# Kernel tuning notes

Hardware: AMD Instinct MI355X
Metric: run time of the kernel (lower is better)

## Reference

```python
import jax, jax.numpy as jnp
from jax import lax
import numpy as np

N, V, P, WE, PE, H, M = 512, 50000, 50, 100, 25, 256, 100
D = WE + PE  # 125, LSTM layer-0 input


def setup_inputs() -> dict:
    key = jax.random.key(0)
    ks = jax.random.split(key, 16)
    s = 0.05  # keep tanh/sigmoid in linear-ish range
    rn = lambda k, shape: jax.random.normal(k, shape, jnp.float32) * s
    return {
        "word_idx": jax.random.randint(ks[0], (N,), 0, V),
        "pos_idx": jax.random.randint(ks[1], (N,), 0, P),
        "word_emb": rn(ks[2], (V, WE)),
        "pos_emb": rn(ks[3], (P, PE)),
        "Wih0": rn(ks[4], (2, 4 * H, D)),
        "Whh0": rn(ks[5], (2, 4 * H, H)),
        "bih0": rn(ks[6], (2, 4 * H)),
        "bhh0": rn(ks[7], (2, 4 * H)),
        "Wih1": rn(ks[8], (2, 4 * H, 2 * H)),
        "Whh1": rn(ks[9], (2, 4 * H, H)),
        "bih1": rn(ks[10], (2, 4 * H)),
        "bhh1": rn(ks[11], (2, 4 * H)),
        "W1": rn(ks[12], (M, 4 * H)),
        "b1": rn(ks[13], (M,)),
        "W2": rn(ks[14], (1, M)),
        "b2": rn(ks[15], (1,)),
    }


def _lstm_dir(x, Wih, Whh, bih, bhh, reverse):
    # x: [n, d_in]; PyTorch gate order i, f, g, o
    Hh = Whh.shape[1]
    xp = jnp.flip(x, 0) if reverse else x
    pre = xp @ Wih.T + (bih + bhh)  # [n, 4H], input contribution precomputed

    def step(carry, p):
        h, c = carry
        g = p + h @ Whh.T
        i, f, gg, o = jnp.split(g, 4)
        c = jax.nn.sigmoid(f) * c + jax.nn.sigmoid(i) * jnp.tanh(gg)
        h = jax.nn.sigmoid(o) * jnp.tanh(c)
        return (h, c), h

    init = (jnp.zeros((Hh,), x.dtype), jnp.zeros((Hh,), x.dtype))
    _, hs = lax.scan(step, init, pre)
    return jnp.flip(hs, 0) if reverse else hs


def _bilstm_layer(x, Wih, Whh, bih, bhh):
    fwd = _lstm_dir(x, Wih[0], Whh[0], bih[0], bhh[0], False)
    bwd = _lstm_dir(x, Wih[1], Whh[1], bih[1], bhh[1], True)
    return jnp.concatenate([fwd, bwd], axis=-1)  # [n, 2H]


def reference(word_idx, pos_idx, word_emb, pos_emb,
              Wih0, Whh0, bih0, bhh0, Wih1, Whh1, bih1, bhh1,
              W1, b1, W2, b2):
    # embedding lookup + concat -> [n, D]
    embeds = jnp.concatenate([word_emb[word_idx], pos_emb[pos_idx]], axis=-1)
    h = _bilstm_layer(embeds, Wih0, Whh0, bih0, bhh0)   # [n, 2H]
    h = _bilstm_layer(h, Wih1, Whh1, bih1, bhh1)        # [n, 2H]
    # Pairwise MLP scorer: score[i, j] = W2 @ tanh(W1 @ cat(h_i, h_j) + b1) + b2
    # Split W1 so we never materialize the [n, n, 4H] concat tensor.
    Hd = h.shape[-1]
    a = h @ W1[:, :Hd].T   # [n, M] head part
    b = h @ W1[:, Hd:].T   # [n, M] dep part
    hid = jnp.tanh(a[:, None, :] + b[None, :, :] + b1)  # [n, n, M]
    scores = jnp.einsum('ijm,m->ij', hid, W2[0]) + b2[0]
    return scores
```

## Files before the change

### kernel.cpp

```cpp
#include <hip/hip_runtime.h>
#include <hip/hip_bf16.h>
#include <stdint.h>


typedef _Float16 f16x2 __attribute__((ext_vector_type(2)));

#define SCOPE_AGENT __HIP_MEMORY_SCOPE_AGENT
constexpr uint32_t SENT = 0x7FFF7FFFu;

__device__ __forceinline__ float fdot2f(uint32_t w, uint32_t h, float acc) {
#if __has_builtin(__builtin_amdgcn_fdot2)
  return __builtin_amdgcn_fdot2(__builtin_bit_cast(f16x2, w),
                                __builtin_bit_cast(f16x2, h), acc, false);
#else
  f16x2 a = __builtin_bit_cast(f16x2, w);
  f16x2 b = __builtin_bit_cast(f16x2, h);
  return acc + (float)a.x * (float)b.x + (float)a.y * (float)b.y;
#endif
}

__device__ __forceinline__ float fsigm(float x) { return 1.f / (1.f + __expf(-x)); }
__device__ __forceinline__ float ftanh(float x) {
  float e = __expf(2.f * x);
  return 1.f - 2.f / (e + 1.f);
}

constexpr size_t ALN(size_t x) { return (x + 1023) & ~(size_t)1023; }
constexpr size_t O_EX    = 0;
constexpr size_t SZ_EX   = 4ull * 512 * 128 * 4;
constexpr size_t O_WPK   = ALN(O_EX + SZ_EX);
constexpr size_t SZ_WPK  = 4ull * 128 * 1024 * 4;
constexpr size_t O_X0    = ALN(O_WPK + SZ_WPK);
constexpr size_t SZ_X0   = 512ull * 125 * 4;
constexpr size_t O_WTIH0 = ALN(O_X0 + SZ_X0);
constexpr size_t SZ_WTIH0 = 2ull * 128 * 1024 * 4;
constexpr size_t O_WTIH1 = ALN(O_WTIH0 + SZ_WTIH0);
constexpr size_t SZ_WTIH1 = 2ull * 512 * 1024 * 4;
constexpr size_t O_WTA   = ALN(O_WTIH1 + SZ_WTIH1);
constexpr size_t SZ_WTAB = 512ull * 100 * 4;
constexpr size_t O_WTB   = ALN(O_WTA + SZ_WTAB);
constexpr size_t O_PRE0  = ALN(O_WTB + SZ_WTAB);
constexpr size_t SZ_PRE  = 2ull * 512 * 1024 * 4;
constexpr size_t O_PRE1  = ALN(O_PRE0 + SZ_PRE);
constexpr size_t O_H0    = ALN(O_PRE1 + SZ_PRE);
constexpr size_t SZ_H    = 512ull * 512 * 4;
constexpr size_t O_H1    = ALN(O_H0 + SZ_H);
constexpr size_t O_AM    = ALN(O_H1 + SZ_H);
constexpr size_t O_BT    = ALN(O_AM + SZ_WTAB);


__global__ void k_init_ex(uint32_t* __restrict__ ex) {
  ex[(size_t)blockIdx.x * 256 + threadIdx.x] = SENT;
}

__global__ void k_embed(const int* __restrict__ wi, const int* __restrict__ pi,
                        const float* __restrict__ we, const float* __restrict__ pe,
                        float* __restrict__ x0) {
  int i = blockIdx.x, k = threadIdx.x;
  if (k < 100)      x0[i * 125 + k] = we[(size_t)wi[i] * 100 + k];
  else if (k < 125) x0[i * 125 + k] = pe[(size_t)pi[i] * 25 + (k - 100)];
}

__global__ void k_transpose(const float* __restrict__ src, int srcRows, int srcCols,
                            int colOff, int colCnt, int dstRows, float* __restrict__ dst) {
  __shared__ float tile[32][33];
  int k0 = blockIdx.x * 32, m0 = blockIdx.y * 32;
  int tx = threadIdx.x, ty = threadIdx.y;
#pragma unroll
  for (int i = 0; i < 4; i++) {
    int m = m0 + ty + i * 8, k = k0 + tx;
    float v = 0.f;
    if (m < srcRows && k < colCnt) v = src[(size_t)m * srcCols + colOff + k];
    tile[ty + i * 8][tx] = v;
  }
  __syncthreads();
#pragma unroll
  for (int i = 0; i < 4; i++) {
    int k = k0 + ty + i * 8, m = m0 + tx;
    if (k < dstRows && m < srcRows) dst[(size_t)k * srcRows + m] = tile[tx][ty + i * 8];
  }
}

__global__ void k_packwhh(const float* __restrict__ whh0, const float* __restrict__ whh1,
                          uint32_t* __restrict__ wpk) {
  int ld = blockIdx.x;
  int kp = blockIdx.y;
  int o  = threadIdx.x;
  const float* W = (ld < 2) ? (whh0 + (size_t)ld * 1024 * 256)
                            : (whh1 + (size_t)(ld - 2) * 1024 * 256);
  int b = o >> 9, t = o & 511;
  int gate = t >> 7, u = t & 127;
  int R = gate * 256 + b * 128 + u;
  f16x2 p;
  p.x = (_Float16)W[(size_t)R * 256 + 2 * kp];
  p.y = (_Float16)W[(size_t)R * 256 + 2 * kp + 1];
  wpk[(size_t)ld * 131072 + (size_t)kp * 1024 + o] = __builtin_bit_cast(uint32_t, p);
}

__global__ __launch_bounds__(256) void k_gemm(
    const float* __restrict__ X, const float* __restrict__ WT,
    const float* __restrict__ bias1, const float* __restrict__ bias2,
    float* __restrict__ out, int Mm, int Nn, int Kpad, int Kreal, int ldx,
    int flipX, int outT) {
  __shared__ float XS[32][64];
  int tid = threadIdx.x;
  int cl = tid & 63, rg = tid >> 6;
  int col = blockIdx.y * 64 + cl;
  int colr = (col < Nn) ? col : (Nn - 1);
  int row0 = blockIdx.x * 32;
  float acc[8];
#pragma unroll
  for (int r = 0; r < 8; r++) acc[r] = 0.f;
  for (int k0 = 0; k0 < Kpad; k0 += 64) {
#pragma unroll
    for (int ii = 0; ii < 8; ii++) {
      int idx = ii * 256 + tid;
      int r = idx >> 6, kk = idx & 63;
      int gr = row0 + r;
      int xr = flipX ? (Mm - 1 - gr) : gr;
      int k = k0 + kk;
      XS[r][kk] = (k < Kreal) ? X[(size_t)xr * ldx + k] : 0.f;
    }
    __syncthreads();
#pragma unroll 4
    for (int kk = 0; kk < 64; kk++) {
      float w = WT[(size_t)(k0 + kk) * Nn + colr];
#pragma unroll
      for (int r = 0; r < 8; r++) acc[r] += XS[rg * 8 + r][kk] * w;
    }
    __syncthreads();
  }
  if (col < Nn) {
    float bb = (bias1 ? bias1[col] : 0.f) + (bias2 ? bias2[col] : 0.f);
#pragma unroll
    for (int r = 0; r < 8; r++) {
      int gr = row0 + rg * 8 + r;
      float v = acc[r] + bb;
      if (outT) out[(size_t)col * Mm + gr] = v;
      else      out[(size_t)gr * Nn + col] = v;
    }
  }
}

__global__ __launch_bounds__(512, 2) void k_lstm(
    const float* __restrict__ preBase, const uint32_t* __restrict__ wpkL,
    float* __restrict__ hout, uint32_t* __restrict__ exL) {
  int d = blockIdx.x >> 1, b = blockIdx.x & 1;
  int t = threadIdx.x;
  int gate = t >> 7, u = t & 127;
  const float* pre = preBase + (size_t)d * 512 * 1024;
  const uint32_t* wsrc = wpkL + (size_t)d * 131072;
  uint32_t* ex = exL + (size_t)d * 512 * 128;

  __shared__ __align__(16) uint32_t h2[128];
  __shared__ float gl[512];
  __shared__ float hh[128];

  uint32_t w[128];
#pragma unroll
  for (int kp = 0; kp < 128; kp++) w[kp] = wsrc[(size_t)kp * 1024 + b * 512 + t];
  if (t < 128) h2[t] = 0u;
  float c = 0.f;
  const int RR = gate * 256 + b * 128 + u;
  __syncthreads();

  float pcur = pre[RR];
  for (int s = 0; s < 512; s++) {
    float pnext = (s < 511) ? pre[(size_t)(s + 1) * 1024 + RR] : 0.f;
    float a0 = pcur, a1 = 0.f, a2 = 0.f, a3 = 0.f;
    const uint4* h4 = (const uint4*)h2;
#pragma unroll
    for (int cc = 0; cc < 32; cc++) {
      uint4 hv = h4[cc];
      a0 = fdot2f(w[4 * cc + 0], hv.x, a0);
      a1 = fdot2f(w[4 * cc + 1], hv.y, a1);
      a2 = fdot2f(w[4 * cc + 2], hv.z, a2);
      a3 = fdot2f(w[4 * cc + 3], hv.w, a3);
    }
    gl[t] = (a0 + a1) + (a2 + a3);
    __syncthreads();
    if (t < 128) {
      float gi = gl[u], gf = gl[128 + u], gg = gl[256 + u], go = gl[384 + u];
      c = fsigm(gf) * c + fsigm(gi) * ftanh(gg);
      float h = fsigm(go) * ftanh(c);
      hh[u] = h;
      int pos = (d == 0) ? s : (511 - s);
      hout[(size_t)pos * 512 + d * 256 + b * 128 + u] = h;
    }
    __syncthreads();
    if (t < 64) {
      f16x2 p;
      p.x = (_Float16)hh[2 * t];
      p.y = (_Float16)hh[2 * t + 1];
      uint32_t pk = __builtin_bit_cast(uint32_t, p);
      h2[b * 64 + t] = pk;
      __hip_atomic_store(&ex[(size_t)s * 128 + b * 64 + t], pk,
                         __ATOMIC_RELAXED, SCOPE_AGENT);
      uint32_t q;
      do {
        q = __hip_atomic_load(&ex[(size_t)s * 128 + (b ^ 1) * 64 + t],
                              __ATOMIC_RELAXED, SCOPE_AGENT);
      } while (__any(q == SENT));
      h2[(b ^ 1) * 64 + t] = q;
    }
    pcur = pnext;
    __syncthreads();
  }
}

__global__ __launch_bounds__(512) void k_score(
    const float* __restrict__ am, const float* __restrict__ bT,
    const float* __restrict__ W2, const float* __restrict__ b2,
    float* __restrict__ out) {
  int i = blockIdx.x;
  int j = threadIdx.x;
  __shared__ float aL[100], w2L[100];
  if (j < 100) { aL[j] = am[(size_t)i * 100 + j]; w2L[j] = W2[j]; }
  __syncthreads();
  float acc = b2[0];
#pragma unroll 4
  for (int m = 0; m < 100; m++)
    acc += w2L[m] * ftanh(aL[m] + bT[(size_t)m * 512 + j]);
  out[(size_t)i * 512 + j] = acc;
}

extern "C" void kernel_launch(void* const* d_in, const int* in_sizes, int n_in,
                              void* d_out, int out_size, void* d_ws, size_t ws_size,
                              hipStream_t stream) {
  const int*   wi   = (const int*)d_in[0];
  const int*   pi   = (const int*)d_in[1];
  const float* we   = (const float*)d_in[2];
  const float* pe   = (const float*)d_in[3];
  const float* Wih0 = (const float*)d_in[4];
  const float* Whh0 = (const float*)d_in[5];
  const float* bih0 = (const float*)d_in[6];
  const float* bhh0 = (const float*)d_in[7];
  const float* Wih1 = (const float*)d_in[8];
  const float* Whh1 = (const float*)d_in[9];
  const float* bih1 = (const float*)d_in[10];
  const float* bhh1 = (const float*)d_in[11];
  const float* W1   = (const float*)d_in[12];
  const float* b1   = (const float*)d_in[13];
  const float* W2   = (const float*)d_in[14];
  const float* b2   = (const float*)d_in[15];

  char* ws = (char*)d_ws;
  uint32_t* ex    = (uint32_t*)(ws + O_EX);
  uint32_t* wpk   = (uint32_t*)(ws + O_WPK);
  float* x0    = (float*)(ws + O_X0);
  float* wtih0 = (float*)(ws + O_WTIH0);
  float* wtih1 = (float*)(ws + O_WTIH1);
  float* wta   = (float*)(ws + O_WTA);
  float* wtb   = (float*)(ws + O_WTB);
  float* pre0  = (float*)(ws + O_PRE0);
  float* pre1  = (float*)(ws + O_PRE1);
  float* h0    = (float*)(ws + O_H0);
  float* h1    = (float*)(ws + O_H1);
  float* am    = (float*)(ws + O_AM);
  float* bt    = (float*)(ws + O_BT);
  float* out   = (float*)d_out;

  k_init_ex<<<1024, 256, 0, stream>>>(ex);

  k_embed<<<512, 128, 0, stream>>>(wi, pi, we, pe, x0);

  dim3 tb(32, 8);
  k_transpose<<<dim3(4, 32),  tb, 0, stream>>>(Wih0,              1024, 125, 0,   125, 128, wtih0);
  k_transpose<<<dim3(4, 32),  tb, 0, stream>>>(Wih0 + 1024 * 125, 1024, 125, 0,   125, 128, wtih0 + 128 * 1024);
  k_transpose<<<dim3(16, 32), tb, 0, stream>>>(Wih1,              1024, 512, 0,   512, 512, wtih1);
  k_transpose<<<dim3(16, 32), tb, 0, stream>>>(Wih1 + 1024 * 512, 1024, 512, 0,   512, 512, wtih1 + 512 * 1024);
  k_transpose<<<dim3(16, 4),  tb, 0, stream>>>(W1,                100, 1024, 0,   512, 512, wta);
  k_transpose<<<dim3(16, 4),  tb, 0, stream>>>(W1,                100, 1024, 512, 512, 512, wtb);

  k_packwhh<<<dim3(4, 128), 1024, 0, stream>>>(Whh0, Whh1, wpk);

  for (int d = 0; d < 2; d++)
    k_gemm<<<dim3(16, 16), 256, 0, stream>>>(x0, wtih0 + (size_t)d * 128 * 1024,
        bih0 + d * 1024, bhh0 + d * 1024, pre0 + (size_t)d * 512 * 1024,
        512, 1024, 128, 125, 125, d, 0);

  k_lstm<<<4, 512, 0, stream>>>(pre0, wpk, h0, ex);

  for (int d = 0; d < 2; d++)
    k_gemm<<<dim3(16, 16), 256, 0, stream>>>(h0, wtih1 + (size_t)d * 512 * 1024,
        bih1 + d * 1024, bhh1 + d * 1024, pre1 + (size_t)d * 512 * 1024,
        512, 1024, 512, 512, 512, d, 0);

  k_lstm<<<4, 512, 0, stream>>>(pre1, wpk + 2 * 131072, h1, ex + 2ull * 512 * 128);

  k_gemm<<<dim3(16, 2), 256, 0, stream>>>(h1, wta, b1, nullptr, am, 512, 100, 512, 512, 512, 0, 0);
  k_gemm<<<dim3(16, 2), 256, 0, stream>>>(h1, wtb, nullptr, nullptr, bt, 512, 100, 512, 512, 512, 0, 1);

  k_score<<<512, 512, 0, stream>>>(am, bt, W2, b2, out);
}
```

Before: 2.467 ms.

## Split LSTM recurrence across eight blocks per direction with shuffle-reduced row dots

The recurrent LSTM kernel now runs 8 blocks of 1024 threads per direction instead of 2 blocks of 512 threads. Each gate row's 256-wide dot product is split across 8 lanes, each holding 16 packed fp16 weight pairs in registers, and the partial sums are combined with xor shuffles. The per-step hidden-state exchange goes through global atomics across the 8 blocks, and the Whh packing kernel is rewritten for the new uint4 layout. The goal is to shorten the serial per-step dot-product chain and reduce register pressure. The cost is a wider cross-block synchronization each timestep and more polling traffic.

```diff
diff --git a/kernel.cpp b/kernel.cpp
--- a/kernel.cpp
+++ b/kernel.cpp
@@ -19,6 +19,13 @@
 #endif
 }
 
+__device__ __forceinline__ uint32_t packpair(float x, float y) {
+  f16x2 p;
+  p.x = (_Float16)x;
+  p.y = (_Float16)y;
+  return __builtin_bit_cast(uint32_t, p);
+}
+
 __device__ __forceinline__ float fsigm(float x) { return 1.f / (1.f + __expf(-x)); }
 __device__ __forceinline__ float ftanh(float x) {
   float e = __expf(2.f * x);
@@ -29,7 +36,7 @@
 constexpr size_t O_EX    = 0;
 constexpr size_t SZ_EX   = 4ull * 512 * 128 * 4;
 constexpr size_t O_WPK   = ALN(O_EX + SZ_EX);
-constexpr size_t SZ_WPK  = 4ull * 128 * 1024 * 4;
+constexpr size_t SZ_WPK  = 4ull * 8 * 4 * 1024 * 16;
 constexpr size_t O_X0    = ALN(O_WPK + SZ_WPK);
 constexpr size_t SZ_X0   = 512ull * 125 * 4;
 constexpr size_t O_WTIH0 = ALN(O_X0 + SZ_X0);
@@ -84,17 +91,21 @@
 __global__ void k_packwhh(const float* __restrict__ whh0, const float* __restrict__ whh1,
                           uint32_t* __restrict__ wpk) {
   int ld = blockIdx.x;
-  int kp = blockIdx.y;
-  int o  = threadIdx.x;
+  int b  = blockIdx.y;
+  int c  = blockIdx.z;
+  int t  = threadIdx.x;
   const float* W = (ld < 2) ? (whh0 + (size_t)ld * 1024 * 256)
                             : (whh1 + (size_t)(ld - 2) * 1024 * 256);
-  int b = o >> 9, t = o & 511;
-  int gate = t >> 7, u = t & 127;
-  int R = gate * 256 + b * 128 + u;
-  f16x2 p;
-  p.x = (_Float16)W[(size_t)R * 256 + 2 * kp];
-  p.y = (_Float16)W[(size_t)R * 256 + 2 * kp + 1];
-  wpk[(size_t)ld * 131072 + (size_t)kp * 1024 + o] = __builtin_bit_cast(uint32_t, p);
+  int rl = t >> 3, kc = t & 7;
+  int g = rl >> 5, ul = rl & 31;
+  int R = g * 256 + b * 32 + ul;
+  const float* src = W + (size_t)R * 256 + kc * 32 + c * 8;
+  uint4 outv;
+  outv.x = packpair(src[0], src[1]);
+  outv.y = packpair(src[2], src[3]);
+  outv.z = packpair(src[4], src[5]);
+  outv.w = packpair(src[6], src[7]);
+  ((uint4*)wpk)[(size_t)ld * 32768 + (size_t)b * 4096 + (size_t)c * 1024 + t] = outv;
 }
 
 __global__ __launch_bounds__(256) void k_gemm(
@@ -142,66 +153,92 @@
   }
 }
 
-__global__ __launch_bounds__(512, 2) void k_lstm(
+__global__ __launch_bounds__(1024)
+__attribute__((amdgpu_waves_per_eu(4, 4)))
+void k_lstm(
     const float* __restrict__ preBase, const uint32_t* __restrict__ wpkL,
     float* __restrict__ hout, uint32_t* __restrict__ exL) {
-  int d = blockIdx.x >> 1, b = blockIdx.x & 1;
+  int d = blockIdx.x >> 3, b = blockIdx.x & 7;
   int t = threadIdx.x;
-  int gate = t >> 7, u = t & 127;
+  int rl = t >> 3, kc = t & 7;
   const float* pre = preBase + (size_t)d * 512 * 1024;
-  const uint32_t* wsrc = wpkL + (size_t)d * 131072;
   uint32_t* ex = exL + (size_t)d * 512 * 128;
+  const uint4* wv = ((const uint4*)wpkL) + (size_t)(d * 8 + b) * 4096;
 
   __shared__ __align__(16) uint32_t h2[128];
-  __shared__ float gl[512];
-  __shared__ float hh[128];
-
-  uint32_t w[128];
-#pragma unroll
-  for (int kp = 0; kp < 128; kp++) w[kp] = wsrc[(size_t)kp * 1024 + b * 512 + t];
+  __shared__ float s1[128];
+
+  uint4 W0 = wv[t];
+  uint4 W1 = wv[1024 + t];
+  uint4 W2 = wv[2048 + t];
+  uint4 W3 = wv[3072 + t];
+#define WPIN(W) asm volatile("" : "+v"(W.x), "+v"(W.y), "+v"(W.z), "+v"(W.w));
+  WPIN(W0) WPIN(W1) WPIN(W2) WPIN(W3)
+#undef WPIN
+
   if (t < 128) h2[t] = 0u;
-  float c = 0.f;
-  const int RR = gate * 256 + b * 128 + u;
+  float cst = 0.f;
+  const int g = rl >> 5, ul = rl & 31;
+  const int RR = g * 256 + b * 32 + ul;
+  const int kc4 = kc * 4;
+  float pcur = (kc == 0) ? pre[RR] : 0.f;
   __syncthreads();
 
-  float pcur = pre[RR];
   for (int s = 0; s < 512; s++) {
-    float pnext = (s < 511) ? pre[(size_t)(s + 1) * 1024 + RR] : 0.f;
+    float pnext = (kc == 0 && s < 511) ? pre[(size_t)(s + 1) * 1024 + RR] : 0.f;
     float a0 = pcur, a1 = 0.f, a2 = 0.f, a3 = 0.f;
     const uint4* h4 = (const uint4*)h2;
-#pragma unroll
-    for (int cc = 0; cc < 32; cc++) {
-      uint4 hv = h4[cc];
-      a0 = fdot2f(w[4 * cc + 0], hv.x, a0);
-      a1 = fdot2f(w[4 * cc + 1], hv.y, a1);
-      a2 = fdot2f(w[4 * cc + 2], hv.z, a2);
-      a3 = fdot2f(w[4 * cc + 3], hv.w, a3);
-    }
-    gl[t] = (a0 + a1) + (a2 + a3);
+    {
+      uint4 hv = h4[kc4 + 0];
+      a0 = fdot2f(W0.x, hv.x, a0); a1 = fdot2f(W0.y, hv.y, a1);
+      a2 = fdot2f(W0.z, hv.z, a2); a3 = fdot2f(W0.w, hv.w, a3);
+    }
+    {
+      uint4 hv = h4[kc4 + 1];
+      a0 = fdot2f(W1.x, hv.x, a0); a1 = fdot2f(W1.y, hv.y, a1);
+      a2 = fdot2f(W1.z, hv.z, a2); a3 = fdot2f(W1.w, hv.w, a3);
+    }
+    {
+      uint4 hv = h4[kc4 + 2];
+      a0 = fdot2f(W2.x, hv.x, a0); a1 = fdot2f(W2.y, hv.y, a1);
+      a2 = fdot2f(W2.z, hv.z, a2); a3 = fdot2f(W2.w, hv.w, a3);
+    }
+    {
+      uint4 hv = h4[kc4 + 3];
+      a0 = fdot2f(W3.x, hv.x, a0); a1 = fdot2f(W3.y, hv.y, a1);
+      a2 = fdot2f(W3.z, hv.z, a2); a3 = fdot2f(W3.w, hv.w, a3);
+    }
+    float p = (a0 + a1) + (a2 + a3);
+    p += __shfl_xor(p, 1);
+    p += __shfl_xor(p, 2);
+    p += __shfl_xor(p, 4);
+    if (kc == 0) s1[rl] = p;
     __syncthreads();
-    if (t < 128) {
-      float gi = gl[u], gf = gl[128 + u], gg = gl[256 + u], go = gl[384 + u];
-      c = fsigm(gf) * c + fsigm(gi) * ftanh(gg);
-      float h = fsigm(go) * ftanh(c);
-      hh[u] = h;
+
+    if (t < 32) {
+      float gi = s1[t], gf = s1[32 + t], gg = s1[64 + t], go = s1[96 + t];
+      cst = fsigm(gf) * cst + fsigm(gi) * ftanh(gg);
+      float h = fsigm(go) * ftanh(cst);
+      float hB = __shfl_down(h, 1);
+      if (!(t & 1)) {
+        uint32_t pk = packpair(h, hB);
+        int j = b * 16 + (t >> 1);
+        __hip_atomic_store(&ex[(size_t)s * 128 + j], pk,
+                           __ATOMIC_RELAXED, SCOPE_AGENT);
+        h2[j] = pk;
+      }
       int pos = (d == 0) ? s : (511 - s);
-      hout[(size_t)pos * 512 + d * 256 + b * 128 + u] = h;
-    }
-    __syncthreads();
-    if (t < 64) {
-      f16x2 p;
-      p.x = (_Float16)hh[2 * t];
-      p.y = (_Float16)hh[2 * t + 1];
-      uint32_t pk = __builtin_bit_cast(uint32_t, p);
-      h2[b * 64 + t] = pk;
-      __hip_atomic_store(&ex[(size_t)s * 128 + b * 64 + t], pk,
-                         __ATOMIC_RELAXED, SCOPE_AGENT);
-      uint32_t q;
-      do {
-        q = __hip_atomic_load(&ex[(size_t)s * 128 + (b ^ 1) * 64 + t],
-                              __ATOMIC_RELAXED, SCOPE_AGENT);
-      } while (__any(q == SENT));
-      h2[(b ^ 1) * 64 + t] = q;
+      hout[(size_t)pos * 512 + d * 256 + b * 32 + t] = h;
+    } else if (t >= 64 && t < 192) {
+      int j2 = t - 64;
+      if ((j2 >> 4) != b) {
+        uint32_t q;
+        do {
+          q = __hip_atomic_load(&ex[(size_t)s * 128 + j2],
+                                __ATOMIC_RELAXED, SCOPE_AGENT);
+        } while (__any(q == SENT));
+        h2[j2] = q;
+      }
     }
     pcur = pnext;
     __syncthreads();
@@ -272,21 +309,21 @@
   k_transpose<<<dim3(16, 4),  tb, 0, stream>>>(W1,                100, 1024, 0,   512, 512, wta);
   k_transpose<<<dim3(16, 4),  tb, 0, stream>>>(W1,                100, 1024, 512, 512, 512, wtb);
 
-  k_packwhh<<<dim3(4, 128), 1024, 0, stream>>>(Whh0, Whh1, wpk);
+  k_packwhh<<<dim3(4, 8, 4), 1024, 0, stream>>>(Whh0, Whh1, wpk);
 
   for (int d = 0; d < 2; d++)
     k_gemm<<<dim3(16, 16), 256, 0, stream>>>(x0, wtih0 + (size_t)d * 128 * 1024,
         bih0 + d * 1024, bhh0 + d * 1024, pre0 + (size_t)d * 512 * 1024,
         512, 1024, 128, 125, 125, d, 0);
 
-  k_lstm<<<4, 512, 0, stream>>>(pre0, wpk, h0, ex);
+  k_lstm<<<16, 1024, 0, stream>>>(pre0, wpk, h0, ex);
 
   for (int d = 0; d < 2; d++)
     k_gemm<<<dim3(16, 16), 256, 0, stream>>>(h0, wtih1 + (size_t)d * 512 * 1024,
         bih1 + d * 1024, bhh1 + d * 1024, pre1 + (size_t)d * 512 * 1024,
         512, 1024, 512, 512, 512, d, 0);
 
-  k_lstm<<<4, 512, 0, stream>>>(pre1, wpk + 2 * 131072, h1, ex + 2ull * 512 * 128);
+  k_lstm<<<16, 1024, 0, stream>>>(pre1, wpk + 2 * 131072, h1, ex + 2ull * 512 * 128);
 
   k_gemm<<<dim3(16, 2), 256, 0, stream>>>(h1, wta, b1, nullptr, am, 512, 100, 512, 512, 512, 0, 0);
   k_gemm<<<dim3(16, 2), 256, 0, stream>>>(h1, wtb, nullptr, nullptr, bt, 512, 100, 512, 512, 512, 0, 1);
```

Measured after the change: 2.549 ms. 1.03x slower.
